# Kernel optimization log

Measured on AMD Instinct MI355X. Metric: run time of the kernel, lower is better.

The kernel has to match this reference:

```python
import jax, jax.numpy as jnp
import numpy as np
import math

B, S, HID = 2, 2048, 1024
NH = 16
HD = HID // NH


def setup_inputs() -> dict:
    key = jax.random.key(0)
    ks = jax.random.split(key, 5)
    std = 1.0 / math.sqrt(HID)
    return {
        "x": jax.random.normal(ks[0], (B, S, HID), dtype=jnp.float32),
        "wq": jax.random.normal(ks[1], (HID, HID), dtype=jnp.float32) * std,
        "wk": jax.random.normal(ks[2], (HID, HID), dtype=jnp.float32) * std,
        "wv": jax.random.normal(ks[3], (HID, HID), dtype=jnp.float32) * std,
        "wo": jax.random.normal(ks[4], (HID, HID), dtype=jnp.float32) * std,
    }


def reference(x, wq, wk, wv, wo):
    # x: [B, S, HID]; weights stored as nn.Linear weight [out, in] -> y = x @ W.T
    b, s, _ = x.shape
    scale = 1.0 / math.sqrt(HD)

    def heads(t):  # [B, S, HID] -> [B, NH, S, HD]
        return t.reshape(b, s, NH, HD).transpose(0, 2, 1, 3)

    q = heads(x @ wq.T)
    k = heads(x @ wk.T)
    v = heads(x @ wv.T)

    # single ring step (cp_size=1): streaming-LSE causal attention
    scores = jnp.einsum("bhqd,bhkd->bhqk", q, k) * scale  # [B, NH, S, S]
    q_idx = jnp.arange(s)[:, None]
    k_idx = jnp.arange(s)[None, :]
    causal_mask = k_idx > q_idx  # [S, S]
    scores = jnp.where(causal_mask, -jnp.inf, scores)

    local_max = jnp.max(scores, axis=-1, keepdims=True)
    exp_scores = jnp.exp(scores - local_max)
    local_sum = jnp.sum(exp_scores, axis=-1, keepdims=True)
    attn_num = jnp.einsum("bhqk,bhkd->bhqd", exp_scores, v)
    attn_out = attn_num / (local_sum + 1e-8)  # [B, NH, S, HD]

    attn_out = attn_out.transpose(0, 2, 1, 3).reshape(b, s, HID)
    return attn_out @ wo.T
```

## Files before the change

kernel.cpp:

```cpp
#include <hip/hip_runtime.h>
#include <hip/hip_bf16.h>

#define S_LEN 2048
#define NHEAD 16
#define HDIM 64
#define HID 1024
#define BATCH 2
#define TSTR 136

typedef __attribute__((ext_vector_type(8))) short s16x8;
typedef __attribute__((ext_vector_type(4))) short s16x4;
typedef __attribute__((ext_vector_type(4))) float f32x4;

__device__ __forceinline__ short f2bf(float f) {
    union { __hip_bfloat16 b; short s; } u;
    u.b = __float2bfloat16(f);
    return u.s;
}
__device__ __forceinline__ float fexp2(float x) {
    return __builtin_amdgcn_exp2f(x);
}
__device__ __forceinline__ f32x4 mfma16(s16x8 a, s16x8 b, f32x4 c) {
    return __builtin_amdgcn_mfma_f32_16x16x32_bf16(a, b, c, 0, 0, 0);
}
__device__ __forceinline__ f32x4 mfma16k16(s16x4 a, s16x4 b, f32x4 c) {
    return __builtin_amdgcn_mfma_f32_16x16x16bf16_1k(a, b, c, 0, 0, 0);
}
__device__ __forceinline__ void gload16(const short* g, short* l) {
    __builtin_amdgcn_global_load_lds(
        (const __attribute__((address_space(1))) void*)g,
        (__attribute__((address_space(3))) void*)l, 16, 0, 0);
}

__global__ __launch_bounds__(256) void convert_kernel(
    const float* __restrict__ x,  const float* __restrict__ wq,
    const float* __restrict__ wk, const float* __restrict__ wv,
    const float* __restrict__ wo,
    short* __restrict__ xb, short* __restrict__ wcat, short* __restrict__ wob)
{
    const int F4X = 1048576, F4W = 262144;
    const int total = F4X + 4 * F4W;
    for (int i = blockIdx.x * blockDim.x + threadIdx.x; i < total;
         i += gridDim.x * blockDim.x) {
        const float4* s; short* d; int off;
        if (i < F4X)              { s = (const float4*)x;  d = xb;             off = i; }
        else if (i < F4X + F4W)   { s = (const float4*)wq; d = wcat;           off = i - F4X; }
        else if (i < F4X + 2*F4W) { s = (const float4*)wk; d = wcat + 1048576; off = i - (F4X + F4W); }
        else if (i < F4X + 3*F4W) { s = (const float4*)wv; d = wcat + 2097152; off = i - (F4X + 2*F4W); }
        else                      { s = (const float4*)wo; d = wob;            off = i - (F4X + 3*F4W); }
        float4 v = s[off];
        s16x4 o4 = { f2bf(v.x), f2bf(v.y), f2bf(v.z), f2bf(v.w) };
        *(s16x4*)(d + (size_t)off * 4) = o4;
    }
}

__global__ __launch_bounds__(256) void qkv_gemm2(
    const short* __restrict__ xb, const short* __restrict__ wcat,
    short* __restrict__ q_ws, short* __restrict__ k_ws, short* __restrict__ vt_ws)
{
    __shared__ union SM {
        struct { short A[128][64]; short B[128][64]; } s;
        short T[128][TSTR];
    } sm;
    const int t = threadIdx.x;
    const int lane = t & 63, w = t >> 6;
    const int g = lane >> 4, r15 = lane & 15;
    const int wm = w >> 1, wn = w & 1;
    const int bid = blockIdx.x;
    const int cx = bid & 7, ii = bid >> 3;
    const int mt = cx * 4 + (ii & 3), nt = ii >> 2;
    const int m0 = mt * 128, n0 = nt * 128;
    const int sel = n0 >> 10;
    const int nr0 = n0 & 1023;
    const short* Ag = (sel == 2) ? (wcat + (size_t)(2048 + nr0) * 1024)
                                 : (xb   + (size_t)m0 * 1024);
    const short* Bg = (sel == 2) ? (xb   + (size_t)m0 * 1024)
                                 : (wcat + (size_t)(sel * 1024 + nr0) * 1024);
    const int lrow = lane >> 3;
    const int scol = ((lane & 7) ^ lrow) * 8;
    const int rsw = r15 & 7;

    f32x4 acc[4][4] = {};

    for (int k0 = 0; k0 < 1024; k0 += 64) {
        __syncthreads();
        #pragma unroll
        for (int ch = 0; ch < 4; ++ch) {
            const int row = w * 32 + ch * 8;
            gload16(Ag + (size_t)(row + lrow) * 1024 + k0 + scol, &sm.s.A[row][0]);
            gload16(Bg + (size_t)(row + lrow) * 1024 + k0 + scol, &sm.s.B[row][0]);
        }
        __syncthreads();
        #pragma unroll
        for (int kk = 0; kk < 2; ++kk) {
            s16x8 af[4], bfr[4];
            #pragma unroll
            for (int mi = 0; mi < 4; ++mi)
                af[mi] = *(const s16x8*)&sm.s.A[wm * 64 + mi * 16 + r15][((kk * 4 + g) ^ rsw) * 8];
            #pragma unroll
            for (int ni = 0; ni < 4; ++ni)
                bfr[ni] = *(const s16x8*)&sm.s.B[wn * 64 + ni * 16 + r15][((kk * 4 + g) ^ rsw) * 8];
            #pragma unroll
            for (int mi = 0; mi < 4; ++mi)
                #pragma unroll
                for (int ni = 0; ni < 4; ++ni)
                    acc[mi][ni] = mfma16(af[mi], bfr[ni], acc[mi][ni]);
        }
    }

    __syncthreads();
    #pragma unroll
    for (int mi = 0; mi < 4; ++mi)
    #pragma unroll
    for (int ni = 0; ni < 4; ++ni)
        #pragma unroll
        for (int reg = 0; reg < 4; ++reg)
            sm.T[wm * 64 + mi * 16 + g * 4 + reg][wn * 64 + ni * 16 + r15]
                = f2bf(acc[mi][ni][reg]);
    __syncthreads();

    const int b = m0 >> 11;
    const int ms = m0 & 2047;
    #pragma unroll
    for (int it = 0; it < 8; ++it) {
        int u = w + it * 4;
        int half = u & 1;
        int rg = u >> 1;
        int r = rg * 8 + lrow;
        int colc = half * 64 + (lane & 7) * 8;
        s16x8 v = *(const s16x8*)&sm.T[r][colc];
        if (sel == 2) {
            int n = nr0 + r;
            int h = n >> 6, d = n & 63;
            *(s16x8*)(vt_ws + ((size_t)(b * NHEAD + h) * HDIM + d) * S_LEN + ms + colc) = v;
        } else {
            int s = ms + r;
            int n = nr0 + colc;
            int h = n >> 6, d = n & 63;
            short* dst = (sel == 0) ? q_ws : k_ws;
            *(s16x8*)(dst + ((size_t)(b * NHEAD + h) * S_LEN + s) * HDIM + d) = v;
        }
    }
}

__global__ __launch_bounds__(256) void attn_kernel2(
    const short* __restrict__ q_ws, const short* __restrict__ k_ws,
    const short* __restrict__ vt_ws, short* __restrict__ attn_ws)
{
    __shared__ short Ks[2][64][64];
    __shared__ short Vts[2][64][64];
    const int t = threadIdx.x;
    const int lane = t & 63, w = t >> 6;
    const int g = lane >> 4, r15 = lane & 15;
    const int bid = blockIdx.x;
    const int lb = (bid & 7) * 64 + (bid >> 3);
    const int p = lb & 15;
    const int bh = lb >> 4;
    const size_t base = (size_t)bh * S_LEN * HDIM;
    const float KSC = 0.18033688f;
    const int swr = (r15 & 7) << 3;
    const int r0 = t >> 3, c0 = (t & 7) * 8;
    const int cx0 = c0 ^ ((r0 & 7) << 3);
    const int b = bh >> 4, h = bh & 15;

    for (int phase = 0; phase < 2; ++phase) {
        const int qt = phase ? (31 - p) : p;
        const int q0 = qt * 64;
        const int ntk = qt + 1;
        const int qg = q0 + w * 16 + r15;
        s16x8 qf0 = *(const s16x8*)(q_ws + base + (size_t)qg * HDIM + g * 8);
        s16x8 qf1 = *(const s16x8*)(q_ws + base + (size_t)qg * HDIM + 32 + g * 8);
        f32x4 o[4] = {};
        float mrun = -1e30f, lrun = 0.f;

        *(s16x8*)&Ks[0][r0][cx0]        = *(const s16x8*)(k_ws  + base + (size_t)r0 * HDIM + c0);
        *(s16x8*)&Ks[0][r0 + 32][cx0]   = *(const s16x8*)(k_ws  + base + (size_t)(r0 + 32) * HDIM + c0);
        *(s16x8*)&Vts[0][r0][cx0]       = *(const s16x8*)(vt_ws + base + (size_t)r0 * S_LEN + c0);
        *(s16x8*)&Vts[0][r0 + 32][cx0]  = *(const s16x8*)(vt_ws + base + (size_t)(r0 + 32) * S_LEN + c0);
        __syncthreads();

        for (int kt = 0; kt < ntk; ++kt) {
            const int cur = kt & 1;
            const bool pre = (kt + 1 < ntk);
            s16x8 ka, kb, va, vb;
            if (pre) {
                const int kn = (kt + 1) * 64;
                ka = *(const s16x8*)(k_ws  + base + (size_t)(kn + r0) * HDIM + c0);
                kb = *(const s16x8*)(k_ws  + base + (size_t)(kn + r0 + 32) * HDIM + c0);
                va = *(const s16x8*)(vt_ws + base + (size_t)r0 * S_LEN + kn + c0);
                vb = *(const s16x8*)(vt_ws + base + (size_t)(r0 + 32) * S_LEN + kn + c0);
            }
            const bool dg = (kt == ntk - 1);
            const int fend = dg ? (w + 1) : 4;

            s16x8 kfa[4][2];
            s16x4 vfa[4][4];
            #pragma unroll
            for (int f = 0; f < 4; ++f)
                if (f < fend)
                    #pragma unroll
                    for (int c = 0; c < 2; ++c)
                        kfa[f][c] = *(const s16x8*)&Ks[cur][f * 16 + r15][(c * 32 + g * 8) ^ swr];
            #pragma unroll
            for (int f2 = 0; f2 < 4; ++f2)
                #pragma unroll
                for (int f = 0; f < 4; ++f)
                    if (f < fend)
                        vfa[f2][f] = *(const s16x4*)&Vts[cur][f2 * 16 + r15][(f * 16 + g * 4) ^ swr];

            float pv[4][4];
            float pmax = -1e30f;
            __builtin_amdgcn_s_setprio(1);
            #pragma unroll
            for (int f = 0; f < 4; ++f)
                if (f < fend) {
                    f32x4 z = { 0.f, 0.f, 0.f, 0.f };
                    z = mfma16(kfa[f][0], qf0, z);
                    z = mfma16(kfa[f][1], qf1, z);
                    #pragma unroll
                    for (int reg = 0; reg < 4; ++reg) {
                        float sv = z[reg] * KSC;
                        if (dg && f == w) sv = (g * 4 + reg > r15) ? -1e30f : sv;
                        pv[f][reg] = sv;
                        pmax = fmaxf(pmax, sv);
                    }
                }
            __builtin_amdgcn_s_setprio(0);
            pmax = fmaxf(pmax, __shfl_xor(pmax, 16));
            pmax = fmaxf(pmax, __shfl_xor(pmax, 32));
            float newm = fmaxf(mrun, pmax);
            float sc = fexp2(mrun - newm);
            float rsum = 0.f;
            s16x4 pb[4];
            #pragma unroll
            for (int f = 0; f < 4; ++f)
                if (f < fend)
                    #pragma unroll
                    for (int reg = 0; reg < 4; ++reg) {
                        float e = fexp2(pv[f][reg] - newm);
                        rsum += e;
                        pb[f][reg] = f2bf(e);
                    }
            rsum += __shfl_xor(rsum, 16);
            rsum += __shfl_xor(rsum, 32);
            lrun = lrun * sc + rsum;
            mrun = newm;
            #pragma unroll
            for (int f2 = 0; f2 < 4; ++f2) o[f2] *= sc;

            __builtin_amdgcn_s_setprio(1);
            #pragma unroll
            for (int f2 = 0; f2 < 4; ++f2)
                #pragma unroll
                for (int f = 0; f < 4; ++f)
                    if (f < fend)
                        o[f2] = mfma16k16(vfa[f2][f], pb[f], o[f2]);
            __builtin_amdgcn_s_setprio(0);

            if (pre) {
                *(s16x8*)&Ks[cur ^ 1][r0][cx0]       = ka;
                *(s16x8*)&Ks[cur ^ 1][r0 + 32][cx0]  = kb;
                *(s16x8*)&Vts[cur ^ 1][r0][cx0]      = va;
                *(s16x8*)&Vts[cur ^ 1][r0 + 32][cx0] = vb;
            }
            __syncthreads();
        }

        float inv = 1.f / (lrun + 1e-8f);
        size_t obase = ((size_t)b * S_LEN + qg) * HID + h * HDIM + g * 4;
        #pragma unroll
        for (int f2 = 0; f2 < 4; ++f2) {
            s16x4 ov = { f2bf(o[f2][0] * inv), f2bf(o[f2][1] * inv),
                         f2bf(o[f2][2] * inv), f2bf(o[f2][3] * inv) };
            *(s16x4*)(attn_ws + obase + f2 * 16) = ov;
        }
    }
}

__global__ __launch_bounds__(256) void wo_gemm2(
    const short* __restrict__ attn, const short* __restrict__ wob,
    float* __restrict__ out)
{
    __shared__ short As[128][64];
    __shared__ short Bs[128][64];
    const int t = threadIdx.x;
    const int lane = t & 63, w = t >> 6;
    const int g = lane >> 4, r15 = lane & 15;
    const int wm = w >> 1, wn = w & 1;
    const int bid = blockIdx.x;
    const int cx = bid & 7, ii = bid >> 3;
    const int mt = cx * 4 + (ii & 3), nt = ii >> 2;
    const int m0 = mt * 128, n0 = nt * 128;
    const int lrow = lane >> 3;
    const int scol = ((lane & 7) ^ lrow) * 8;
    const int rsw = r15 & 7;

    f32x4 acc[4][4] = {};

    for (int k0 = 0; k0 < 1024; k0 += 64) {
        __syncthreads();
        #pragma unroll
        for (int ch = 0; ch < 4; ++ch) {
            const int row = w * 32 + ch * 8;
            gload16(attn + (size_t)(m0 + row + lrow) * 1024 + k0 + scol, &As[row][0]);
            gload16(wob  + (size_t)(n0 + row + lrow) * 1024 + k0 + scol, &Bs[row][0]);
        }
        __syncthreads();
        #pragma unroll
        for (int kk = 0; kk < 2; ++kk) {
            s16x8 af[4], bfr[4];
            #pragma unroll
            for (int mi = 0; mi < 4; ++mi)
                af[mi] = *(const s16x8*)&As[wm * 64 + mi * 16 + r15][((kk * 4 + g) ^ rsw) * 8];
            #pragma unroll
            for (int ni = 0; ni < 4; ++ni)
                bfr[ni] = *(const s16x8*)&Bs[wn * 64 + ni * 16 + r15][((kk * 4 + g) ^ rsw) * 8];
            #pragma unroll
            for (int mi = 0; mi < 4; ++mi)
                #pragma unroll
                for (int ni = 0; ni < 4; ++ni)
                    acc[mi][ni] = mfma16(af[mi], bfr[ni], acc[mi][ni]);
        }
    }

    #pragma unroll
    for (int mi = 0; mi < 4; ++mi)
    #pragma unroll
    for (int ni = 0; ni < 4; ++ni) {
        #pragma unroll
        for (int reg = 0; reg < 4; ++reg) {
            int m = m0 + wm * 64 + mi * 16 + g * 4 + reg;
            int n = n0 + wn * 64 + ni * 16 + r15;
            out[(size_t)m * 1024 + n] = acc[mi][ni][reg];
        }
    }
}

extern "C" void kernel_launch(void* const* d_in, const int* in_sizes, int n_in,
                              void* d_out, int out_size, void* d_ws, size_t ws_size,
                              hipStream_t stream) {
    const float* x  = (const float*)d_in[0];
    const float* wq = (const float*)d_in[1];
    const float* wk = (const float*)d_in[2];
    const float* wv = (const float*)d_in[3];
    const float* wo = (const float*)d_in[4];
    float* out = (float*)d_out;

    const size_t ELEMS = (size_t)BATCH * S_LEN * HID;
    short* q_ws    = (short*)d_ws;
    short* k_ws    = q_ws + ELEMS;
    short* vt_ws   = k_ws + ELEMS;
    short* xb      = vt_ws + ELEMS;
    short* attn_ws = xb;
    short* wcat    = xb + ELEMS;
    short* wob     = wcat + 3145728;

    convert_kernel<<<dim3(2048), dim3(256), 0, stream>>>(x, wq, wk, wv, wo, xb, wcat, wob);
    qkv_gemm2<<<dim3(768), dim3(256), 0, stream>>>(xb, wcat, q_ws, k_ws, vt_ws);
    attn_kernel2<<<dim3(512), dim3(256), 0, stream>>>(q_ws, k_ws, vt_ws, attn_ws);
    wo_gemm2<<<dim3(256), dim3(256), 0, stream>>>(attn_ws, wob, out);
}
```

Before: 124.7 us.

## Restructure attention inner loop with lazy rescale, K32 PV MFMA, deferred row-sum

Reworks the flash-attention inner loop. Online-softmax rescaling now happens only when the tile max exceeds the running max by more than a threshold (wave-uniform check), and the row-sum reduction across lanes is deferred to the end. The PV product switches from 16x16x16 to 16x16x32 bf16 MFMAs by packing probabilities with a cheap round-to-nearest bit pack, and the diagonal tile now computes all four fragments and masks instead of branching per fragment. It also strength-reduces the prefetch address arithmetic. The risk is extra work on diagonal tiles and possible overflow or precision drift from the lazy max threshold.

Measured after the change: 120.4 us. 1.04x faster.

```diff
diff --git a/kernel.cpp b/kernel.cpp
--- a/kernel.cpp
+++ b/kernel.cpp
@@ -23,13 +23,15 @@
 __device__ __forceinline__ f32x4 mfma16(s16x8 a, s16x8 b, f32x4 c) {
     return __builtin_amdgcn_mfma_f32_16x16x32_bf16(a, b, c, 0, 0, 0);
 }
-__device__ __forceinline__ f32x4 mfma16k16(s16x4 a, s16x4 b, f32x4 c) {
-    return __builtin_amdgcn_mfma_f32_16x16x16bf16_1k(a, b, c, 0, 0, 0);
-}
 __device__ __forceinline__ void gload16(const short* g, short* l) {
     __builtin_amdgcn_global_load_lds(
         (const __attribute__((address_space(1))) void*)g,
         (__attribute__((address_space(3))) void*)l, 16, 0, 0);
+}
+__device__ __forceinline__ unsigned bfpack(float a, float b) {
+    unsigned ua = __builtin_bit_cast(unsigned, a) + 0x8000u;
+    unsigned ub = __builtin_bit_cast(unsigned, b) + 0x8000u;
+    return (ub & 0xFFFF0000u) | (ua >> 16);
 }
 
 __global__ __launch_bounds__(256) void convert_kernel(
@@ -162,16 +164,20 @@
     const int r0 = t >> 3, c0 = (t & 7) * 8;
     const int cx0 = c0 ^ ((r0 & 7) << 3);
     const int b = bh >> 4, h = bh & 15;
+    const int qloc = w * 16 + r15;
+
+    union P8 { unsigned u[4]; s16x8 v; };
+    union V8 { s16x4 h[2]; s16x8 v; };
 
     for (int phase = 0; phase < 2; ++phase) {
         const int qt = phase ? (31 - p) : p;
         const int q0 = qt * 64;
         const int ntk = qt + 1;
-        const int qg = q0 + w * 16 + r15;
+        const int qg = q0 + qloc;
         s16x8 qf0 = *(const s16x8*)(q_ws + base + (size_t)qg * HDIM + g * 8);
         s16x8 qf1 = *(const s16x8*)(q_ws + base + (size_t)qg * HDIM + 32 + g * 8);
         f32x4 o[4] = {};
-        float mrun = -1e30f, lrun = 0.f;
+        float mrun = -1e30f, lrun_p = 0.f;
 
         *(s16x8*)&Ks[0][r0][cx0]        = *(const s16x8*)(k_ws  + base + (size_t)r0 * HDIM + c0);
         *(s16x8*)&Ks[0][r0 + 32][cx0]   = *(const s16x8*)(k_ws  + base + (size_t)(r0 + 32) * HDIM + c0);
@@ -179,82 +185,92 @@
         *(s16x8*)&Vts[0][r0 + 32][cx0]  = *(const s16x8*)(vt_ws + base + (size_t)(r0 + 32) * S_LEN + c0);
         __syncthreads();
 
+        const short* kpa = k_ws  + base + (size_t)(64 + r0) * HDIM + c0;
+        const short* kpb = kpa + 32 * HDIM;
+        const short* vpa = vt_ws + base + (size_t)r0 * S_LEN + 64 + c0;
+        const short* vpb = vpa + 32 * S_LEN;
+
         for (int kt = 0; kt < ntk; ++kt) {
             const int cur = kt & 1;
             const bool pre = (kt + 1 < ntk);
+            const bool dg = (kt == ntk - 1);
             s16x8 ka, kb, va, vb;
             if (pre) {
-                const int kn = (kt + 1) * 64;
-                ka = *(const s16x8*)(k_ws  + base + (size_t)(kn + r0) * HDIM + c0);
-                kb = *(const s16x8*)(k_ws  + base + (size_t)(kn + r0 + 32) * HDIM + c0);
-                va = *(const s16x8*)(vt_ws + base + (size_t)r0 * S_LEN + kn + c0);
-                vb = *(const s16x8*)(vt_ws + base + (size_t)(r0 + 32) * S_LEN + kn + c0);
-            }
-            const bool dg = (kt == ntk - 1);
-            const int fend = dg ? (w + 1) : 4;
+                ka = *(const s16x8*)kpa;  kb = *(const s16x8*)kpb;
+                va = *(const s16x8*)vpa;  vb = *(const s16x8*)vpb;
+                kpa += 64 * HDIM; kpb += 64 * HDIM; vpa += 64; vpb += 64;
+            }
 
             s16x8 kfa[4][2];
-            s16x4 vfa[4][4];
             #pragma unroll
             for (int f = 0; f < 4; ++f)
-                if (f < fend)
+                #pragma unroll
+                for (int c = 0; c < 2; ++c)
+                    kfa[f][c] = *(const s16x8*)&Ks[cur][f * 16 + r15][(c * 32 + g * 8) ^ swr];
+            V8 vfr[4][2];
+            #pragma unroll
+            for (int f2 = 0; f2 < 4; ++f2)
+                #pragma unroll
+                for (int kc = 0; kc < 2; ++kc) {
+                    vfr[f2][kc].h[0] = *(const s16x4*)&Vts[cur][f2 * 16 + r15][(kc * 32 + g * 4) ^ swr];
+                    vfr[f2][kc].h[1] = *(const s16x4*)&Vts[cur][f2 * 16 + r15][(kc * 32 + 16 + g * 4) ^ swr];
+                }
+
+            f32x4 z[4];
+            __builtin_amdgcn_s_setprio(1);
+            #pragma unroll
+            for (int f = 0; f < 4; ++f) {
+                f32x4 zz = { 0.f, 0.f, 0.f, 0.f };
+                zz = mfma16(kfa[f][0], qf0, zz);
+                zz = mfma16(kfa[f][1], qf1, zz);
+                z[f] = zz;
+            }
+            __builtin_amdgcn_s_setprio(0);
+
+            if (dg) {
+                #pragma unroll
+                for (int f = 0; f < 4; ++f)
                     #pragma unroll
-                    for (int c = 0; c < 2; ++c)
-                        kfa[f][c] = *(const s16x8*)&Ks[cur][f * 16 + r15][(c * 32 + g * 8) ^ swr];
-            #pragma unroll
-            for (int f2 = 0; f2 < 4; ++f2)
-                #pragma unroll
-                for (int f = 0; f < 4; ++f)
-                    if (f < fend)
-                        vfa[f2][f] = *(const s16x4*)&Vts[cur][f2 * 16 + r15][(f * 16 + g * 4) ^ swr];
-
-            float pv[4][4];
-            float pmax = -1e30f;
+                    for (int reg = 0; reg < 4; ++reg)
+                        if (f * 16 + g * 4 + reg > qloc) z[f][reg] = -3e30f;
+            }
+
+            float zf[4];
+            #pragma unroll
+            for (int f = 0; f < 4; ++f)
+                zf[f] = fmaxf(fmaxf(z[f][0], z[f][1]), fmaxf(z[f][2], z[f][3]));
+            float zm = fmaxf(fmaxf(zf[0], zf[1]), fmaxf(zf[2], zf[3]));
+            zm = fmaxf(zm, __shfl_xor(zm, 16));
+            zm = fmaxf(zm, __shfl_xor(zm, 32));
+            float pm = zm * KSC;
+
+            if (!__all(pm - mrun <= 8.0f)) {
+                float newm = fmaxf(mrun, pm);
+                float sc = fexp2(mrun - newm);
+                #pragma unroll
+                for (int f2 = 0; f2 < 4; ++f2) o[f2] *= sc;
+                lrun_p *= sc;
+                mrun = newm;
+            }
+
+            P8 p8[2];
+            #pragma unroll
+            for (int f = 0; f < 4; ++f) {
+                float e0 = fexp2(__builtin_fmaf(z[f][0], KSC, -mrun));
+                float e1 = fexp2(__builtin_fmaf(z[f][1], KSC, -mrun));
+                float e2 = fexp2(__builtin_fmaf(z[f][2], KSC, -mrun));
+                float e3 = fexp2(__builtin_fmaf(z[f][3], KSC, -mrun));
+                lrun_p += (e0 + e1) + (e2 + e3);
+                p8[f >> 1].u[(f & 1) * 2]     = bfpack(e0, e1);
+                p8[f >> 1].u[(f & 1) * 2 + 1] = bfpack(e2, e3);
+            }
+
             __builtin_amdgcn_s_setprio(1);
             #pragma unroll
-            for (int f = 0; f < 4; ++f)
-                if (f < fend) {
-                    f32x4 z = { 0.f, 0.f, 0.f, 0.f };
-                    z = mfma16(kfa[f][0], qf0, z);
-                    z = mfma16(kfa[f][1], qf1, z);
-                    #pragma unroll
-                    for (int reg = 0; reg < 4; ++reg) {
-                        float sv = z[reg] * KSC;
-                        if (dg && f == w) sv = (g * 4 + reg > r15) ? -1e30f : sv;
-                        pv[f][reg] = sv;
-                        pmax = fmaxf(pmax, sv);
-                    }
-                }
-            __builtin_amdgcn_s_setprio(0);
-            pmax = fmaxf(pmax, __shfl_xor(pmax, 16));
-            pmax = fmaxf(pmax, __shfl_xor(pmax, 32));
-            float newm = fmaxf(mrun, pmax);
-            float sc = fexp2(mrun - newm);
-            float rsum = 0.f;
-            s16x4 pb[4];
-            #pragma unroll
-            for (int f = 0; f < 4; ++f)
-                if (f < fend)
-                    #pragma unroll
-                    for (int reg = 0; reg < 4; ++reg) {
-                        float e = fexp2(pv[f][reg] - newm);
-                        rsum += e;
-                        pb[f][reg] = f2bf(e);
-                    }
-            rsum += __shfl_xor(rsum, 16);
-            rsum += __shfl_xor(rsum, 32);
-            lrun = lrun * sc + rsum;
-            mrun = newm;
-            #pragma unroll
-            for (int f2 = 0; f2 < 4; ++f2) o[f2] *= sc;
-
-            __builtin_amdgcn_s_setprio(1);
-            #pragma unroll
-            for (int f2 = 0; f2 < 4; ++f2)
-                #pragma unroll
-                for (int f = 0; f < 4; ++f)
-                    if (f < fend)
-                        o[f2] = mfma16k16(vfa[f2][f], pb[f], o[f2]);
+            for (int f2 = 0; f2 < 4; ++f2) {
+                o[f2] = mfma16(vfr[f2][0].v, p8[0].v, o[f2]);
+                o[f2] = mfma16(vfr[f2][1].v, p8[1].v, o[f2]);
+            }
             __builtin_amdgcn_s_setprio(0);
 
             if (pre) {
@@ -266,7 +282,10 @@
             __syncthreads();
         }
 
-        float inv = 1.f / (lrun + 1e-8f);
+        float lr = lrun_p;
+        lr += __shfl_xor(lr, 16);
+        lr += __shfl_xor(lr, 32);
+        float inv = 1.f / (lr + 1e-8f);
         size_t obase = ((size_t)b * S_LEN + qg) * HID + h * HDIM + g * 4;
         #pragma unroll
         for (int f2 = 0; f2 < 4; ++f2) {
```
